# Performance work log

Hardware: AMD Instinct MI355X
Metric: run time of the kernel (lower is better)

The kernel has to match this reference:

```python
import jax, jax.numpy as jnp
import numpy as np

NUM_OPS = 8
D = 1024
B = 8192


def setup_inputs() -> dict:
    key = jax.random.key(0)
    k1, k2, k3, k4 = jax.random.split(key, 4)
    x = jax.random.normal(k1, (B, D), dtype=jnp.float32)
    logits = 0.001 * jax.random.normal(k2, (NUM_OPS,), dtype=jnp.float32)
    Ws = jax.random.normal(k3, (NUM_OPS, D, D), dtype=jnp.float32) * (1.0 / np.sqrt(D))
    bs = jax.random.normal(k4, (NUM_OPS, D), dtype=jnp.float32) * 0.01
    return {"x": x, "logits": logits, "Ws": Ws, "bs": bs, "num_on_samples": 2}


def reference(x, logits, Ws, bs, num_on_samples):
    # non_stochastic_call: top-k op selection by architecture logits,
    # dispatch x to the selected ops, sum-combine the results.
    _, top_k_ids = jax.lax.top_k(logits, num_on_samples)  # [k]
    W_sel = jnp.take(Ws, top_k_ids, axis=0)  # [k, D, D]
    b_sel = jnp.take(bs, top_k_ids, axis=0)  # [k, D]
    # each op is Dense(D->D) + relu: [k, B, D]
    op_results = jax.nn.relu(jnp.einsum('bd,kde->kbe', x, W_sel) + b_sel[:, None, :])
    return jnp.sum(op_results, axis=0)  # [B, D]
```

## Files before the change

### kernel.cpp

```cpp
#include <hip/hip_runtime.h>
#include <hip/hip_bf16.h>

#define NUM_OPS 8
#define D 1024
#define B_ROWS 8192

typedef unsigned short ushort_t;
typedef __attribute__((ext_vector_type(8))) short bf16x8;
typedef __attribute__((ext_vector_type(4))) float f32x4;
typedef __attribute__((ext_vector_type(4))) float float4v;
typedef __attribute__((ext_vector_type(8))) unsigned short ushort8;

__device__ __forceinline__ unsigned short f2bf(float f) {
    union { float f; unsigned int u; } v; v.f = f;
    unsigned int u = v.u;
    unsigned int lsb = (u >> 16) & 1u;
    u += 0x7fffu + lsb;
    return (unsigned short)(u >> 16);
}

__device__ __forceinline__ void load_lds16(const void* g, void* l) {
    __builtin_amdgcn_global_load_lds(
        (const __attribute__((address_space(1))) void*)g,
        (__attribute__((address_space(3))) void*)l,
        16, 0, 0);
}

__device__ __forceinline__ void top2(const float* __restrict__ logits, int& i0, int& i1) {
    float best = -__builtin_inff(); i0 = 0;
    for (int i = 0; i < NUM_OPS; ++i) { float v = logits[i]; if (v > best) { best = v; i0 = i; } }
    float best2 = -__builtin_inff(); i1 = 0;
    for (int i = 0; i < NUM_OPS; ++i) {
        if (i == i0) continue;
        float v = logits[i]; if (v > best2) { best2 = v; i1 = i; }
    }
}

__global__ void convert_x(const float* __restrict__ x, ushort_t* __restrict__ xb) {
    int i = (blockIdx.x * 256 + threadIdx.x) * 8;
    float4v v0 = *(const float4v*)(x + i);
    float4v v1 = *(const float4v*)(x + i + 4);
    ushort8 o;
    o[0] = f2bf(v0[0]); o[1] = f2bf(v0[1]); o[2] = f2bf(v0[2]); o[3] = f2bf(v0[3]);
    o[4] = f2bf(v1[0]); o[5] = f2bf(v1[1]); o[6] = f2bf(v1[2]); o[7] = f2bf(v1[3]);
    *(ushort8*)(xb + i) = o;
}

__global__ void gather_transpose_W(const float* __restrict__ Ws,
                                   const float* __restrict__ logits,
                                   ushort_t* __restrict__ Wt) {
    __shared__ float t[32][33];
    int i0, i1; top2(logits, i0, i1);
    int e    = blockIdx.x >> 10;
    int tile = blockIdx.x & 1023;
    int td = (tile >> 5) << 5;
    int te = (tile & 31) << 5;
    int tx = threadIdx.x & 31, ty = threadIdx.x >> 5;
    const float* W = Ws + (size_t)(e ? i1 : i0) * D * D;
    for (int r = 0; r < 4; ++r)
        t[ty + 8 * r][tx] = W[(size_t)(td + ty + 8 * r) * D + te + tx];
    __syncthreads();
    ushort_t* o = Wt + (size_t)e * D * D;
    for (int r = 0; r < 4; ++r)
        o[(size_t)(te + ty + 8 * r) * D + td + tx] = f2bf(t[tx][ty + 8 * r]);
}

__device__ __forceinline__ void stageA(const ushort_t* __restrict__ xbf, int brow,
                                       int u, ushort_t* dst, int tid) {
    #pragma unroll
    for (int q = 0; q < 4; ++q) {
        const int c   = q * 512 + tid;
        const int rr  = c >> 3;
        const int gcb = ((c & 7) * 16) ^ ((rr & 7) << 4);
        load_lds16(xbf + (size_t)(brow + rr) * D + u * 64 + (gcb >> 1), dst + c * 8);
    }
}
__device__ __forceinline__ void stageB(const ushort_t* __restrict__ Wt, int bcol,
                                       int u, ushort_t* dst, int tid) {
    #pragma unroll
    for (int q = 0; q < 2; ++q) {
        const int c   = q * 512 + tid;
        const int e   = c >> 9, cc = c & 511;
        const int n   = cc >> 3;
        const int gcb = ((cc & 7) * 16) ^ ((n & 7) << 4);
        load_lds16(Wt + (size_t)e * D * D + (size_t)(bcol + n) * D + u * 64 + (gcb >> 1),
                   dst + c * 8);
    }
}

#define SB()    __builtin_amdgcn_sched_barrier(0)
#define PRIO1() __builtin_amdgcn_s_setprio(1)
#define PRIO0() __builtin_amdgcn_s_setprio(0)
#define VM0()   do { asm volatile("s_waitcnt vmcnt(0)" ::: "memory"); } while (0)

#define READF(AF, BF, CA, CB)                                                      \
    do {                                                                           \
        _Pragma("unroll") for (int kk = 0; kk < 2; ++kk)                           \
        _Pragma("unroll") for (int m = 0; m < 4; ++m)                              \
            AF[kk][m] = *(const bf16x8*)((const char*)(CA) +                       \
                (size_t)((rgrp * 64 + m * 16 + l15) * 128) + (kk ? x1 : x0));      \
        _Pragma("unroll") for (int e = 0; e < 2; ++e)                              \
        _Pragma("unroll") for (int kk = 0; kk < 2; ++kk)                           \
        _Pragma("unroll") for (int n16 = 0; n16 < 2; ++n16)                        \
            BF[e][kk][n16] = *(const bf16x8*)((const char*)(CB) + e * 8192 +       \
                (size_t)((cgrp * 32 + n16 * 16 + l15) * 128) + (kk ? x1 : x0));    \
    } while (0)

#define MM32(AF, BF)                                                               \
    do {                                                                           \
        PRIO1();                                                                   \
        _Pragma("unroll") for (int kk = 0; kk < 2; ++kk)                           \
        _Pragma("unroll") for (int e = 0; e < 2; ++e)                              \
        _Pragma("unroll") for (int m = 0; m < 4; ++m)                              \
        _Pragma("unroll") for (int n16 = 0; n16 < 2; ++n16)                        \
            acc[e][m][n16] = __builtin_amdgcn_mfma_f32_16x16x32_bf16(              \
                AF[kk][m], BF[e][kk][n16], acc[e][m][n16], 0, 0, 0);               \
        PRIO0();                                                                   \
    } while (0)

#define TILE(FR_A, FR_B, SLOT_RA, SLOT_RB, FC_A, FC_B, SU, DA, DB, DORD, DOSTG)    \
    do {                                                                           \
        VM0();                                                                     \
        __builtin_amdgcn_s_barrier();                                              \
        if (DORD) READF(FR_A, FR_B, SLOT_RA, SLOT_RB);                             \
        if (DOSTG) { stageA(xbf, brow, (SU), DA, tid);                             \
                     stageB(Wt,  bcol, (SU), DB, tid); }                           \
        SB();                                                                      \
        MM32(FC_A, FC_B);                                                          \
    } while (0)

__global__ __launch_bounds__(512, 2)
void gemm_dual(const ushort_t* __restrict__ xbf, const ushort_t* __restrict__ Wt,
               const float* __restrict__ bs, const float* __restrict__ logits,
               float* __restrict__ out) {
    __shared__ __align__(16) ushort_t As0[256 * 64], As1[256 * 64], As2[256 * 64];
    __shared__ __align__(16) ushort_t Bs0[2 * 64 * 64], Bs1[2 * 64 * 64], Bs2[2 * 64 * 64];

    const int tid  = threadIdx.x;
    const int wv   = tid >> 6;
    const int lane = tid & 63;
    const int rgrp = wv >> 1, cgrp = wv & 1;
    const int l15  = lane & 15, lq = lane >> 4;
    const int swz  = (l15 & 7) << 4;
    const int x0   = (lq * 16) ^ swz;
    const int x1   = (64 + lq * 16) ^ swz;

    const int bid  = blockIdx.x;
    const int brow = (bid & 31) * 256;
    const int bcol = (bid >> 5) * 64;

    f32x4 acc[2][4][2] = {};
    bf16x8 a0[2][4], b0[2][2][2];
    bf16x8 a1[2][4], b1[2][2][2];

    stageA(xbf, brow, 0, As0, tid); stageB(Wt, bcol, 0, Bs0, tid);
    stageA(xbf, brow, 1, As1, tid); stageB(Wt, bcol, 1, Bs1, tid);
    SB();
    asm volatile("s_waitcnt vmcnt(6)" ::: "memory");
    __builtin_amdgcn_s_barrier();
    READF(a0, b0, As0, Bs0);
    SB();

    TILE(a1, b1, As1, Bs1, a0, b0,  2, As2, Bs2, true,  true);
    TILE(a0, b0, As2, Bs2, a1, b1,  3, As0, Bs0, true,  true);
    TILE(a1, b1, As0, Bs0, a0, b0,  4, As1, Bs1, true,  true);
    TILE(a0, b0, As1, Bs1, a1, b1,  5, As2, Bs2, true,  true);
    TILE(a1, b1, As2, Bs2, a0, b0,  6, As0, Bs0, true,  true);
    TILE(a0, b0, As0, Bs0, a1, b1,  7, As1, Bs1, true,  true);
    TILE(a1, b1, As1, Bs1, a0, b0,  8, As2, Bs2, true,  true);
    TILE(a0, b0, As2, Bs2, a1, b1,  9, As0, Bs0, true,  true);
    TILE(a1, b1, As0, Bs0, a0, b0, 10, As1, Bs1, true,  true);
    TILE(a0, b0, As1, Bs1, a1, b1, 11, As2, Bs2, true,  true);
    TILE(a1, b1, As2, Bs2, a0, b0, 12, As0, Bs0, true,  true);
    TILE(a0, b0, As0, Bs0, a1, b1, 13, As1, Bs1, true,  true);
    TILE(a1, b1, As1, Bs1, a0, b0, 14, As2, Bs2, true,  true);
    TILE(a0, b0, As2, Bs2, a1, b1, 15, As0, Bs0, true,  true);
    TILE(a1, b1, As0, Bs0, a0, b0,  0, As0, Bs0, true,  false);
    TILE(a0, b0, As0, Bs0, a1, b1,  0, As0, Bs0, false, false);

    int i0, i1; top2(logits, i0, i1);
    #pragma unroll
    for (int n16 = 0; n16 < 2; ++n16) {
        const int col = bcol + cgrp * 32 + n16 * 16 + l15;
        const float bb0 = bs[i0 * D + col];
        const float bb1 = bs[i1 * D + col];
        #pragma unroll
        for (int m = 0; m < 4; ++m) {
            const int rbase = brow + rgrp * 64 + m * 16 + lq * 4;
            #pragma unroll
            for (int i = 0; i < 4; ++i) {
                float v0 = acc[0][m][n16][i] + bb0; v0 = v0 > 0.f ? v0 : 0.f;
                float v1 = acc[1][m][n16][i] + bb1; v1 = v1 > 0.f ? v1 : 0.f;
                out[(size_t)(rbase + i) * D + col] = v0 + v1;
            }
        }
    }
}

extern "C" void kernel_launch(void* const* d_in, const int* in_sizes, int n_in,
                              void* d_out, int out_size, void* d_ws, size_t ws_size,
                              hipStream_t stream) {
    const float* x      = (const float*)d_in[0];
    const float* logits = (const float*)d_in[1];
    const float* Ws     = (const float*)d_in[2];
    const float* bs     = (const float*)d_in[3];
    float* out = (float*)d_out;

    char* ws = (char*)d_ws;
    ushort_t* xbf = (ushort_t*)ws;
    ushort_t* Wt  = (ushort_t*)(ws + (size_t)B_ROWS * D * 2);

    convert_x<<<(B_ROWS * D) / (256 * 8), 256, 0, stream>>>(x, xbf);
    gather_transpose_W<<<2 * (D / 32) * (D / 32), 256, 0, stream>>>(Ws, logits, Wt);

    gemm_dual<<<512, 512, 0, stream>>>(xbf, Wt, bs, logits, out);
}
```

Measured before the change: 53.99 us.

## Merge prep kernels and hand-schedule LDS fragment reads with partial lgkmcnt waits

Fuses the x-to-bf16 conversion and the W gather/transpose into one launch, removing a kernel boundary. In the GEMM main loop, fragment reads become explicit inline-asm ds_read_b128 with immediate offsets into named register sets. A partial lgkmcnt(15) wait lets the MFMAs on the previous set start while the next set's LDS reads are still in flight. This depends on manual waitcnt correctness, because the compiler cannot track the LDS reads issued through inline asm, and it may raise register pressure.

New measurement: 49.06 us. 1.1x faster.

```diff
diff --git a/kernel.cpp b/kernel.cpp
--- a/kernel.cpp
+++ b/kernel.cpp
@@ -36,33 +36,38 @@
     }
 }
 
-__global__ void convert_x(const float* __restrict__ x, ushort_t* __restrict__ xb) {
-    int i = (blockIdx.x * 256 + threadIdx.x) * 8;
-    float4v v0 = *(const float4v*)(x + i);
-    float4v v1 = *(const float4v*)(x + i + 4);
-    ushort8 o;
-    o[0] = f2bf(v0[0]); o[1] = f2bf(v0[1]); o[2] = f2bf(v0[2]); o[3] = f2bf(v0[3]);
-    o[4] = f2bf(v1[0]); o[5] = f2bf(v1[1]); o[6] = f2bf(v1[2]); o[7] = f2bf(v1[3]);
-    *(ushort8*)(xb + i) = o;
-}
-
-__global__ void gather_transpose_W(const float* __restrict__ Ws,
-                                   const float* __restrict__ logits,
-                                   ushort_t* __restrict__ Wt) {
+__global__ void prep_kernel(const float* __restrict__ x,
+                            const float* __restrict__ Ws,
+                            const float* __restrict__ logits,
+                            ushort_t* __restrict__ xbf,
+                            ushort_t* __restrict__ Wt) {
     __shared__ float t[32][33];
-    int i0, i1; top2(logits, i0, i1);
-    int e    = blockIdx.x >> 10;
-    int tile = blockIdx.x & 1023;
-    int td = (tile >> 5) << 5;
-    int te = (tile & 31) << 5;
-    int tx = threadIdx.x & 31, ty = threadIdx.x >> 5;
-    const float* W = Ws + (size_t)(e ? i1 : i0) * D * D;
-    for (int r = 0; r < 4; ++r)
-        t[ty + 8 * r][tx] = W[(size_t)(td + ty + 8 * r) * D + te + tx];
-    __syncthreads();
-    ushort_t* o = Wt + (size_t)e * D * D;
-    for (int r = 0; r < 4; ++r)
-        o[(size_t)(te + ty + 8 * r) * D + td + tx] = f2bf(t[tx][ty + 8 * r]);
+    const int bid = blockIdx.x;
+    const int tid = threadIdx.x;
+    if (bid < 4096) {
+        int i = (bid * 256 + tid) * 8;
+        float4v v0 = *(const float4v*)(x + i);
+        float4v v1 = *(const float4v*)(x + i + 4);
+        ushort8 o;
+        o[0] = f2bf(v0[0]); o[1] = f2bf(v0[1]); o[2] = f2bf(v0[2]); o[3] = f2bf(v0[3]);
+        o[4] = f2bf(v1[0]); o[5] = f2bf(v1[1]); o[6] = f2bf(v1[2]); o[7] = f2bf(v1[3]);
+        *(ushort8*)(xbf + i) = o;
+    } else {
+        int i0, i1; top2(logits, i0, i1);
+        const int b  = bid - 4096;
+        const int e    = b >> 10;
+        const int tile = b & 1023;
+        const int td = (tile >> 5) << 5;
+        const int te = (tile & 31) << 5;
+        const int tx = tid & 31, ty = tid >> 5;
+        const float* W = Ws + (size_t)(e ? i1 : i0) * D * D;
+        for (int r = 0; r < 4; ++r)
+            t[ty + 8 * r][tx] = W[(size_t)(td + ty + 8 * r) * D + te + tx];
+        __syncthreads();
+        ushort_t* o = Wt + (size_t)e * D * D;
+        for (int r = 0; r < 4; ++r)
+            o[(size_t)(te + ty + 8 * r) * D + td + tx] = f2bf(t[tx][ty + 8 * r]);
+    }
 }
 
 __device__ __forceinline__ void stageA(const ushort_t* __restrict__ xbf, int brow,
@@ -91,42 +96,57 @@
 #define SB()    __builtin_amdgcn_sched_barrier(0)
 #define PRIO1() __builtin_amdgcn_s_setprio(1)
 #define PRIO0() __builtin_amdgcn_s_setprio(0)
-#define VM0()   do { asm volatile("s_waitcnt vmcnt(0)" ::: "memory"); } while (0)
-
-#define READF(AF, BF, CA, CB)                                                      \
-    do {                                                                           \
-        _Pragma("unroll") for (int kk = 0; kk < 2; ++kk)                           \
-        _Pragma("unroll") for (int m = 0; m < 4; ++m)                              \
-            AF[kk][m] = *(const bf16x8*)((const char*)(CA) +                       \
-                (size_t)((rgrp * 64 + m * 16 + l15) * 128) + (kk ? x1 : x0));      \
-        _Pragma("unroll") for (int e = 0; e < 2; ++e)                              \
-        _Pragma("unroll") for (int kk = 0; kk < 2; ++kk)                           \
-        _Pragma("unroll") for (int n16 = 0; n16 < 2; ++n16)                        \
-            BF[e][kk][n16] = *(const bf16x8*)((const char*)(CB) + e * 8192 +       \
-                (size_t)((cgrp * 32 + n16 * 16 + l15) * 128) + (kk ? x1 : x0));    \
+#define VMW(N)  do { asm volatile("s_waitcnt vmcnt(" #N ")" ::: "memory"); SB(); } while (0)
+#define LGW(N)  do { asm volatile("s_waitcnt lgkmcnt(" #N ")" ::: "memory"); SB(); } while (0)
+#define BAR()   do { __builtin_amdgcn_s_barrier(); SB(); } while (0)
+
+#define DSR(dst, addr, imm)                                                    \
+    asm volatile("ds_read_b128 %0, %1 offset:" #imm : "=v"(dst) : "v"(addr))
+
+#define ISSUE_DS(P, SA, SBB)                                                   \
+    do {                                                                       \
+        unsigned aA0 = (unsigned)(size_t)(SA) + aro + x0;                      \
+        unsigned aA1 = (unsigned)(size_t)(SA) + aro + x1;                      \
+        unsigned aB0 = (unsigned)(size_t)(SBB) + bro + x0;                     \
+        unsigned aB1 = (unsigned)(size_t)(SBB) + bro + x1;                     \
+        DSR(P##a0, aA0, 0);    DSR(P##a1, aA0, 2048);                          \
+        DSR(P##a2, aA0, 4096); DSR(P##a3, aA0, 6144);                          \
+        DSR(P##a4, aA1, 0);    DSR(P##a5, aA1, 2048);                          \
+        DSR(P##a6, aA1, 4096); DSR(P##a7, aA1, 6144);                          \
+        DSR(P##b0, aB0, 0);    DSR(P##b1, aB0, 2048);                          \
+        DSR(P##b4, aB0, 8192); DSR(P##b5, aB0, 10240);                         \
+        DSR(P##b2, aB1, 0);    DSR(P##b3, aB1, 2048);                          \
+        DSR(P##b6, aB1, 8192); DSR(P##b7, aB1, 10240);                         \
     } while (0)
 
-#define MM32(AF, BF)                                                               \
-    do {                                                                           \
-        PRIO1();                                                                   \
-        _Pragma("unroll") for (int kk = 0; kk < 2; ++kk)                           \
-        _Pragma("unroll") for (int e = 0; e < 2; ++e)                              \
-        _Pragma("unroll") for (int m = 0; m < 4; ++m)                              \
-        _Pragma("unroll") for (int n16 = 0; n16 < 2; ++n16)                        \
-            acc[e][m][n16] = __builtin_amdgcn_mfma_f32_16x16x32_bf16(              \
-                AF[kk][m], BF[e][kk][n16], acc[e][m][n16], 0, 0, 0);               \
-        PRIO0();                                                                   \
+#define MF(a, b, c) __builtin_amdgcn_mfma_f32_16x16x32_bf16(a, b, c, 0, 0, 0)
+#define Q(P, A, B, E, M, N) acc[E][M][N] = MF(P##A, P##B, acc[E][M][N])
+
+#define MFMA_SET(P)                                                            \
+    do {                                                                       \
+        PRIO1();                                                               \
+        Q(P,a0,b0,0,0,0); Q(P,a0,b1,0,0,1); Q(P,a0,b4,1,0,0); Q(P,a0,b5,1,0,1);\
+        Q(P,a1,b0,0,1,0); Q(P,a1,b1,0,1,1); Q(P,a1,b4,1,1,0); Q(P,a1,b5,1,1,1);\
+        Q(P,a2,b0,0,2,0); Q(P,a2,b1,0,2,1); Q(P,a2,b4,1,2,0); Q(P,a2,b5,1,2,1);\
+        Q(P,a3,b0,0,3,0); Q(P,a3,b1,0,3,1); Q(P,a3,b4,1,3,0); Q(P,a3,b5,1,3,1);\
+        Q(P,a4,b2,0,0,0); Q(P,a4,b3,0,0,1); Q(P,a4,b6,1,0,0); Q(P,a4,b7,1,0,1);\
+        Q(P,a5,b2,0,1,0); Q(P,a5,b3,0,1,1); Q(P,a5,b6,1,1,0); Q(P,a5,b7,1,1,1);\
+        Q(P,a6,b2,0,2,0); Q(P,a6,b3,0,2,1); Q(P,a6,b6,1,2,0); Q(P,a6,b7,1,2,1);\
+        Q(P,a7,b2,0,3,0); Q(P,a7,b3,0,3,1); Q(P,a7,b6,1,3,0); Q(P,a7,b7,1,3,1);\
+        PRIO0();                                                               \
     } while (0)
 
-#define TILE(FR_A, FR_B, SLOT_RA, SLOT_RB, FC_A, FC_B, SU, DA, DB, DORD, DOSTG)    \
-    do {                                                                           \
-        VM0();                                                                     \
-        __builtin_amdgcn_s_barrier();                                              \
-        if (DORD) READF(FR_A, FR_B, SLOT_RA, SLOT_RB);                             \
-        if (DOSTG) { stageA(xbf, brow, (SU), DA, tid);                             \
-                     stageB(Wt,  bcol, (SU), DB, tid); }                           \
-        SB();                                                                      \
-        MM32(FC_A, FC_B);                                                          \
+#define TILE(SETN, SA, SBB, SU, DA, DB, SETC, DOSTG)                           \
+    do {                                                                       \
+        VMW(0);                                                                \
+        BAR();                                                                 \
+        ISSUE_DS(SETN, SA, SBB);                                               \
+        if (DOSTG) { stageA(xbf, brow, (SU), DA, tid);                         \
+                     stageB(Wt,  bcol, (SU), DB, tid); }                       \
+        SB();                                                                  \
+        LGW(15);                                                               \
+        MFMA_SET(SETC);                                                        \
+        SB();                                                                  \
     } while (0)
 
 __global__ __launch_bounds__(512, 2)
@@ -144,39 +164,46 @@
     const int swz  = (l15 & 7) << 4;
     const int x0   = (lq * 16) ^ swz;
     const int x1   = (64 + lq * 16) ^ swz;
+    const unsigned aro = (unsigned)((rgrp * 64 + l15) * 128);
+    const unsigned bro = (unsigned)((cgrp * 32 + l15) * 128);
 
     const int bid  = blockIdx.x;
     const int brow = (bid & 31) * 256;
     const int bcol = (bid >> 5) * 64;
 
     f32x4 acc[2][4][2] = {};
-    bf16x8 a0[2][4], b0[2][2][2];
-    bf16x8 a1[2][4], b1[2][2][2];
+
+    bf16x8 Xa0, Xa1, Xa2, Xa3, Xa4, Xa5, Xa6, Xa7;
+    bf16x8 Xb0, Xb1, Xb2, Xb3, Xb4, Xb5, Xb6, Xb7;
+    bf16x8 Ya0, Ya1, Ya2, Ya3, Ya4, Ya5, Ya6, Ya7;
+    bf16x8 Yb0, Yb1, Yb2, Yb3, Yb4, Yb5, Yb6, Yb7;
 
     stageA(xbf, brow, 0, As0, tid); stageB(Wt, bcol, 0, Bs0, tid);
     stageA(xbf, brow, 1, As1, tid); stageB(Wt, bcol, 1, Bs1, tid);
     SB();
-    asm volatile("s_waitcnt vmcnt(6)" ::: "memory");
-    __builtin_amdgcn_s_barrier();
-    READF(a0, b0, As0, Bs0);
+    VMW(6);
+    BAR();
+    ISSUE_DS(X, As0, Bs0);
     SB();
 
-    TILE(a1, b1, As1, Bs1, a0, b0,  2, As2, Bs2, true,  true);
-    TILE(a0, b0, As2, Bs2, a1, b1,  3, As0, Bs0, true,  true);
-    TILE(a1, b1, As0, Bs0, a0, b0,  4, As1, Bs1, true,  true);
-    TILE(a0, b0, As1, Bs1, a1, b1,  5, As2, Bs2, true,  true);
-    TILE(a1, b1, As2, Bs2, a0, b0,  6, As0, Bs0, true,  true);
-    TILE(a0, b0, As0, Bs0, a1, b1,  7, As1, Bs1, true,  true);
-    TILE(a1, b1, As1, Bs1, a0, b0,  8, As2, Bs2, true,  true);
-    TILE(a0, b0, As2, Bs2, a1, b1,  9, As0, Bs0, true,  true);
-    TILE(a1, b1, As0, Bs0, a0, b0, 10, As1, Bs1, true,  true);
-    TILE(a0, b0, As1, Bs1, a1, b1, 11, As2, Bs2, true,  true);
-    TILE(a1, b1, As2, Bs2, a0, b0, 12, As0, Bs0, true,  true);
-    TILE(a0, b0, As0, Bs0, a1, b1, 13, As1, Bs1, true,  true);
-    TILE(a1, b1, As1, Bs1, a0, b0, 14, As2, Bs2, true,  true);
-    TILE(a0, b0, As2, Bs2, a1, b1, 15, As0, Bs0, true,  true);
-    TILE(a1, b1, As0, Bs0, a0, b0,  0, As0, Bs0, true,  false);
-    TILE(a0, b0, As0, Bs0, a1, b1,  0, As0, Bs0, false, false);
+    TILE(Y, As1, Bs1,  2, As2, Bs2, X, true);
+    TILE(X, As2, Bs2,  3, As0, Bs0, Y, true);
+    TILE(Y, As0, Bs0,  4, As1, Bs1, X, true);
+    TILE(X, As1, Bs1,  5, As2, Bs2, Y, true);
+    TILE(Y, As2, Bs2,  6, As0, Bs0, X, true);
+    TILE(X, As0, Bs0,  7, As1, Bs1, Y, true);
+    TILE(Y, As1, Bs1,  8, As2, Bs2, X, true);
+    TILE(X, As2, Bs2,  9, As0, Bs0, Y, true);
+    TILE(Y, As0, Bs0, 10, As1, Bs1, X, true);
+    TILE(X, As1, Bs1, 11, As2, Bs2, Y, true);
+    TILE(Y, As2, Bs2, 12, As0, Bs0, X, true);
+    TILE(X, As0, Bs0, 13, As1, Bs1, Y, true);
+    TILE(Y, As1, Bs1, 14, As2, Bs2, X, true);
+    TILE(X, As2, Bs2, 15, As0, Bs0, Y, true);
+    TILE(Y, As0, Bs0,  0, As0, Bs0, X, false);
+    LGW(0);
+    MFMA_SET(Y);
+    SB();
 
     int i0, i1; top2(logits, i0, i1);
     #pragma unroll
@@ -210,8 +237,6 @@
     ushort_t* xbf = (ushort_t*)ws;
     ushort_t* Wt  = (ushort_t*)(ws + (size_t)B_ROWS * D * 2);
 
-    convert_x<<<(B_ROWS * D) / (256 * 8), 256, 0, stream>>>(x, xbf);
-    gather_transpose_W<<<2 * (D / 32) * (D / 32), 256, 0, stream>>>(Ws, logits, Wt);
-
+    prep_kernel<<<4096 + 2048, 256, 0, stream>>>(x, Ws, logits, xbf, Wt);
     gemm_dual<<<512, 512, 0, stream>>>(xbf, Wt, bs, logits, out);
 }
```
